# Performance work log

Hardware: AMD Instinct MI355X
Metric: run time of the kernel (lower is better)

The kernel has to match this reference:

```python
import jax, jax.numpy as jnp
import numpy as np

B, C, T, F = 16, 64, 500, 32
G = 8
GF = F // G            # 4 freqs per group
OC = GF * 64           # per-group hidden size = 256
IN = GF * C            # per-group input size = 256


def setup_inputs() -> dict:
    key = jax.random.key(0)
    k1, k2, k3, k4, k5 = jax.random.split(key, 5)
    scale = 1.0 / np.sqrt(OC)
    return {
        "x": jax.random.normal(k1, (B, C, T, F), dtype=jnp.float32),
        "weight_ih": jax.random.normal(k2, (G, 3 * OC, IN), dtype=jnp.float32) * scale,
        "weight_hh": jax.random.normal(k3, (G, 3 * OC, OC), dtype=jnp.float32) * scale,
        "bias_ih": jax.random.normal(k4, (G, 3 * OC), dtype=jnp.float32) * scale,
        "bias_hh": jax.random.normal(k5, (G, 3 * OC), dtype=jnp.float32) * scale,
    }


def reference(x, weight_ih, weight_hh, bias_ih, bias_hh):
    b, c, t, f = x.shape
    g = weight_ih.shape[0]
    oc = weight_ih.shape[1] // 3
    gf = f // g
    # [B,C,T,F] -> [B,T,F,C] -> [B,T,G,gf*C]
    xi = jnp.transpose(x, (0, 2, 3, 1)).reshape(b, t, g, gf * c)
    # input projection for all timesteps at once: [B,T,G,3*OC]
    ih = jnp.einsum('btgi,goi->btgo', xi, weight_ih) + bias_ih

    h0 = jnp.zeros((b, g, oc), dtype=x.dtype)

    def step(h, ih_t):
        hh = jnp.einsum('bgo,gpo->bgp', h, weight_hh) + bias_hh
        ri, zi, ni = jnp.split(ih_t, 3, axis=-1)
        rh, zh, nh = jnp.split(hh, 3, axis=-1)
        r = jax.nn.sigmoid(ri + rh)
        z = jax.nn.sigmoid(zi + zh)
        n = jnp.tanh(ni + r * nh)
        h_new = (1 - z) * n + z * h
        return h_new, h_new

    h_last, hs = jax.lax.scan(step, h0, jnp.swapaxes(ih, 0, 1))  # hs: [T,B,G,OC]
    out = jnp.transpose(hs, (1, 0, 2, 3))                # [B,T,G,OC]
    out = out.reshape(b, t, g, gf, oc // gf)             # unflatten OC -> (gf, out_ch)
    out = out.reshape(b, t, f, oc // gf)                 # merge (G,gf) -> F
    out = jnp.transpose(out, (0, 3, 1, 2))               # [B,out_ch,T,F]
    return out, h_last
```

## Files before the change

kernel.cpp:

```cpp
#include <hip/hip_runtime.h>

typedef _Float16 f16;
typedef _Float16 f16x2 __attribute__((ext_vector_type(2)));
typedef _Float16 f16x4 __attribute__((ext_vector_type(4)));
typedef _Float16 f16x8 __attribute__((ext_vector_type(8)));
typedef float    f32x4 __attribute__((ext_vector_type(4)));

#if defined(__has_builtin)
#if __has_builtin(__builtin_amdgcn_fdot2)
#define HAVE_FDOT2 1
#endif
#endif

__device__ __forceinline__ float dot8(f16x8 a, f16x8 b, float acc) {
#ifdef HAVE_FDOT2
  acc = __builtin_amdgcn_fdot2(__builtin_shufflevector(a, a, 0, 1),
                               __builtin_shufflevector(b, b, 0, 1), acc, false);
  acc = __builtin_amdgcn_fdot2(__builtin_shufflevector(a, a, 2, 3),
                               __builtin_shufflevector(b, b, 2, 3), acc, false);
  acc = __builtin_amdgcn_fdot2(__builtin_shufflevector(a, a, 4, 5),
                               __builtin_shufflevector(b, b, 4, 5), acc, false);
  acc = __builtin_amdgcn_fdot2(__builtin_shufflevector(a, a, 6, 7),
                               __builtin_shufflevector(b, b, 6, 7), acc, false);
#else
  #pragma unroll
  for (int i = 0; i < 8; i++) acc += (float)a[i] * (float)b[i];
#endif
  return acc;
}

__global__ void k_pack_x(const float* __restrict__ x, f16* __restrict__ xi) {
  const int tc = blockIdx.x;
  const int b  = blockIdx.y;
  const int t0 = tc * 4;
  const int tid = threadIdx.x;
  __shared__ __align__(16) float lds[64 * 133];
  #pragma unroll
  for (int it = 0; it < 32; it++) {
    int flat = it * 256 + tid;
    int c = flat >> 7;
    int t = (flat >> 5) & 3;
    int f = flat & 31;
    lds[c * 133 + t * 33 + f] =
        x[(((size_t)b * 64 + c) * 500 + t0 + t) * 32 + f];
  }
  __syncthreads();
  const int w = tid >> 6, l = tid & 63;
  #pragma unroll
  for (int rr = 0; rr < 8; rr++) {
    int row = w * 8 + rr;
    int g = row >> 2, t = row & 3;
    f16x4 v;
    #pragma unroll
    for (int e = 0; e < 4; e++) {
      int i = l * 4 + e;
      int gf = i >> 6, c = i & 63;
      v[e] = (f16)lds[c * 133 + t * 33 + g * 4 + gf];
    }
    *(f16x4*)&xi[((size_t)g * 8000 + (size_t)b * 500 + t0 + t) * 256 + l * 4] = v;
  }
}

__global__ void k_pack_wih(const float* __restrict__ w, f16* __restrict__ wh) {
  size_t i0 = ((size_t)blockIdx.x * 256 + threadIdx.x) * 8;
  f32x4 a = *(const f32x4*)(w + i0);
  f32x4 b = *(const f32x4*)(w + i0 + 4);
  f16x8 v;
  v[0]=(f16)a[0]; v[1]=(f16)a[1]; v[2]=(f16)a[2]; v[3]=(f16)a[3];
  v[4]=(f16)b[0]; v[5]=(f16)b[1]; v[6]=(f16)b[2]; v[7]=(f16)b[3];
  *(f16x8*)(wh + i0) = v;
}

__global__ void k_pack_whh(const float* __restrict__ w, f16* __restrict__ wp) {
  const int j = blockIdx.x;
  const int g = blockIdx.y;
  const int tid = threadIdx.x;
  const int row = (tid % 192) * 4 + (j >> 3);
  const int kb  = (tid / 192) * 64 + (j & 7) * 8;
  const float* src = w + ((size_t)g * 768 + row) * 256 + kb;
  f16x8 v;
  #pragma unroll
  for (int e = 0; e < 8; e++) v[e] = (f16)src[e];
  *(f16x8*)&wp[(((size_t)g * 32 + j) * 768 + tid) * 8] = v;
}

__global__ __launch_bounds__(256) void k_gemm(const f16* __restrict__ xi,
                                              const f16* __restrict__ wih,
                                              const float* __restrict__ bias,
                                              f16* __restrict__ ih) {
  const int mt = blockIdx.x;
  const int nt = blockIdx.y;
  const int g  = blockIdx.z;
  const int tid = threadIdx.x;
  const int w = tid >> 6, l = tid & 63;
  __shared__ __align__(16) f16 Als[64 * 64];
  __shared__ __align__(16) f16 Bls[128 * 64];
  f32x4 zero = {0.f, 0.f, 0.f, 0.f};
  f32x4 acc[4][2];
  #pragma unroll
  for (int mi = 0; mi < 4; mi++)
    #pragma unroll
    for (int ni = 0; ni < 2; ni++) acc[mi][ni] = zero;

  const int arow = tid >> 2, aq = tid & 3;
  const int brow = tid >> 1, bq = tid & 1;
  for (int kk = 0; kk < 4; kk++) {
    const f16* asrc = xi + ((size_t)g * 8000 + mt * 64 + arow) * 256 + kk * 64 + aq * 16;
    f16x8 a0 = *(const f16x8*)asrc;
    f16x8 a1 = *(const f16x8*)(asrc + 8);
    *(f16x8*)&Als[arow * 64 + ((aq * 2 + 0) ^ (arow & 7)) * 8] = a0;
    *(f16x8*)&Als[arow * 64 + ((aq * 2 + 1) ^ (arow & 7)) * 8] = a1;
    const f16* bsrc = wih + ((size_t)g * 768 + nt * 128 + brow) * 256 + kk * 64 + bq * 32;
    #pragma unroll
    for (int jj = 0; jj < 4; jj++) {
      f16x8 v = *(const f16x8*)(bsrc + jj * 8);
      *(f16x8*)&Bls[brow * 64 + ((bq * 4 + jj) ^ (brow & 7)) * 8] = v;
    }
    __syncthreads();
    #pragma unroll
    for (int ks = 0; ks < 2; ks++) {
      f16x8 af[4], bf[2];
      #pragma unroll
      for (int mi = 0; mi < 4; mi++) {
        int r = mi * 16 + (l & 15);
        af[mi] = *(const f16x8*)&Als[r * 64 + ((ks * 4 + (l >> 4)) ^ (r & 7)) * 8];
      }
      #pragma unroll
      for (int ni = 0; ni < 2; ni++) {
        int r = w * 32 + ni * 16 + (l & 15);
        bf[ni] = *(const f16x8*)&Bls[r * 64 + ((ks * 4 + (l >> 4)) ^ (r & 7)) * 8];
      }
      #pragma unroll
      for (int mi = 0; mi < 4; mi++)
        #pragma unroll
        for (int ni = 0; ni < 2; ni++)
          acc[mi][ni] = __builtin_amdgcn_mfma_f32_16x16x32_f16(af[mi], bf[ni], acc[mi][ni], 0, 0, 0);
    }
    __syncthreads();
  }
  #pragma unroll
  for (int ni = 0; ni < 2; ni++) {
    int col = nt * 128 + w * 32 + ni * 16 + (l & 15);
    float bs = bias[g * 768 + col];
    #pragma unroll
    for (int mi = 0; mi < 4; mi++) {
      int m0 = mt * 64 + mi * 16 + (l >> 4) * 4;
      #pragma unroll
      for (int e = 0; e < 4; e++) {
        ih[((size_t)g * 8000 + m0 + e) * 768 + col] = (f16)(acc[mi][ni][e] + bs);
      }
    }
  }
}

__global__ __launch_bounds__(768, 3) void k_recur(const f16* __restrict__ ih,
                                                  const f16* __restrict__ wp,
                                                  const float* __restrict__ bias_hh,
                                                  f16* __restrict__ hs,
                                                  float* __restrict__ hlast) {
  const int g = blockIdx.x;
  const int b = blockIdx.y;
  const int tid = threadIdx.x;
  const int kc = tid / 192;
  const int rg = tid % 192;
  __shared__ __align__(16) f16 hsm[256];
  __shared__ __align__(16) float partial[4][768];

  f16x8 wv[32];
  {
    const f16x8* src = (const f16x8*)(wp + (size_t)g * 32 * 768 * 8);
    #pragma unroll
    for (int j = 0; j < 32; j++) wv[j] = src[(size_t)j * 768 + tid];
  }
  float bh_r = 0.f, bh_z = 0.f, bh_n = 0.f;
  if (tid < 256) {
    bh_r = bias_hh[g * 768 + tid];
    bh_z = bias_hh[g * 768 + 256 + tid];
    bh_n = bias_hh[g * 768 + 512 + tid];
    hsm[tid] = (f16)0.f;
  }
  const f16* ihb = ih + ((size_t)g * 8000 + (size_t)b * 500) * 768;
  f16* hsp = hs + (size_t)(b * 8 + g) * 500 * 256;
  f16 ri = (f16)0.f, zi = (f16)0.f, nii = (f16)0.f;
  if (tid < 256) { ri = ihb[tid]; zi = ihb[256 + tid]; nii = ihb[512 + tid]; }
  __syncthreads();

  for (int t = 0; t < 500; t++) {
    f16 rin = ri, zin = zi, nin = nii;
    if (tid < 256 && t + 1 < 500) {
      const f16* p = ihb + (size_t)(t + 1) * 768;
      rin = p[tid]; zin = p[256 + tid]; nin = p[512 + tid];
    }
    float a0 = 0.f, a1 = 0.f, a2 = 0.f, a3 = 0.f;
    const f16x8* hv = (const f16x8*)(hsm + kc * 64);
    #pragma unroll
    for (int jj = 0; jj < 8; jj++) {
      f16x8 h8 = hv[jj];
      a0 = dot8(wv[jj],      h8, a0);
      a1 = dot8(wv[8 + jj],  h8, a1);
      a2 = dot8(wv[16 + jj], h8, a2);
      a3 = dot8(wv[24 + jj], h8, a3);
    }
    f32x4 p4; p4[0] = a0; p4[1] = a1; p4[2] = a2; p4[3] = a3;
    *(f32x4*)&partial[kc][rg * 4] = p4;
    __syncthreads();
    if (tid < 256) {
      const int o = tid;
      float rh = partial[0][o] + partial[1][o] + partial[2][o] + partial[3][o] + bh_r;
      float zh = partial[0][256 + o] + partial[1][256 + o] + partial[2][256 + o] + partial[3][256 + o] + bh_z;
      float nh = partial[0][512 + o] + partial[1][512 + o] + partial[2][512 + o] + partial[3][512 + o] + bh_n;
      float r = 1.f / (1.f + __expf(-((float)ri + rh)));
      float z = 1.f / (1.f + __expf(-((float)zi + zh)));
      float nx = (float)nii + r * nh;
      float n = 2.f / (1.f + __expf(-2.f * nx)) - 1.f;
      float hp = (float)hsm[o];
      float hn = (1.f - z) * n + z * hp;
      hsm[o] = (f16)hn;
      hsp[(size_t)t * 256 + o] = (f16)hn;
    }
    __syncthreads();
    ri = rin; zi = zin; nii = nin;
  }
  if (tid < 256) hlast[(size_t)(b * 8 + g) * 256 + tid] = (float)hsm[tid];
}

__global__ void k_untr(const f16* __restrict__ hs, float* __restrict__ out) {
  const int tc = blockIdx.x;
  const int b  = blockIdx.y;
  const int t0 = tc * 8;
  const int tid = threadIdx.x;
  __shared__ __align__(16) f16 lds[8 * 8 * 260];
  {
    const int row = tid >> 2, q = tid & 3;
    const int g = row >> 3, tt = row & 7;
    if (t0 + tt < 500) {
      const f16* src = hs + (((size_t)b * 8 + g) * 500 + t0 + tt) * 256 + q * 64;
      #pragma unroll
      for (int jj = 0; jj < 16; jj++) {
        *(f16x4*)&lds[(tt * 8 + g) * 260 + q * 64 + jj * 4] = *(const f16x4*)(src + jj * 4);
      }
    }
  }
  __syncthreads();
  const int w = tid >> 6, l = tid & 63;
  const int tt2 = w * 2 + (l >> 5);
  const int f = l & 31;
  const int gg = f >> 2, gf = f & 3;
  if (t0 + tt2 < 500) {
    float* dst = out + (((size_t)b * 64) * 500 + t0 + tt2) * 32 + f;
    const f16* srcl = &lds[(tt2 * 8 + gg) * 260 + gf * 64];
    #pragma unroll 4
    for (int och = 0; och < 64; och++) {
      dst[(size_t)och * 500 * 32] = (float)srcl[och];
    }
  }
}

extern "C" void kernel_launch(void* const* d_in, const int* in_sizes, int n_in,
                              void* d_out, int out_size, void* d_ws, size_t ws_size,
                              hipStream_t stream) {
  const float* x   = (const float*)d_in[0];
  const float* wih = (const float*)d_in[1];
  const float* whh = (const float*)d_in[2];
  const float* bih = (const float*)d_in[3];
  const float* bhh = (const float*)d_in[4];
  float* out   = (float*)d_out;
  float* hlast = out + 16384000;

  char* ws = (char*)d_ws;
  f16* ih_h  = (f16*)(ws);
  f16* xi_h  = (f16*)(ws + 98304000);
  f16* wih_h = (f16*)(ws + 131072000);
  f16* whh_p = (f16*)(ws + 134217728);
  f16* hs_h  = (f16*)(ws + 137363456);

  k_pack_x  <<<dim3(125, 16), 256, 0, stream>>>(x, xi_h);
  k_pack_wih<<<768, 256, 0, stream>>>(wih, wih_h);
  k_pack_whh<<<dim3(32, 8), 768, 0, stream>>>(whh, whh_p);
  k_gemm    <<<dim3(125, 6, 8), 256, 0, stream>>>(xi_h, wih_h, bih, ih_h);
  k_recur   <<<dim3(8, 16), 768, 0, stream>>>(ih_h, whh_p, bhh, hs_h, hlast);
  k_untr    <<<dim3(63, 16), 256, 0, stream>>>(hs_h, out);
}
```

Measured before the change: 682.4 us.

## Use MFMA for recurrent hidden matvec and drop cross-chunk partial reduction

The recurrent kernel now computes h·W_hh with 16x16x32 f16 MFMA instructions instead of fdot2. Only one row of each tile is used, because every row of the A operand is fed the same hidden vector. Each wave owns full-K output columns, so the four-way LDS partial-sum reduction is gone. The block shrinks from 768 to 512 threads, and W_hh is repacked into the MFMA B-operand fragment layout. The previous hidden state stays in an fp32 register instead of being reread from f16 LDS. The trade-off is that 15/16 of the MFMA work is wasted, and the per-step chain of dependent MFMAs adds latency.

```diff
diff --git a/kernel.cpp b/kernel.cpp
--- a/kernel.cpp
+++ b/kernel.cpp
@@ -1,33 +1,9 @@
 #include <hip/hip_runtime.h>
 
 typedef _Float16 f16;
-typedef _Float16 f16x2 __attribute__((ext_vector_type(2)));
 typedef _Float16 f16x4 __attribute__((ext_vector_type(4)));
 typedef _Float16 f16x8 __attribute__((ext_vector_type(8)));
 typedef float    f32x4 __attribute__((ext_vector_type(4)));
-
-#if defined(__has_builtin)
-#if __has_builtin(__builtin_amdgcn_fdot2)
-#define HAVE_FDOT2 1
-#endif
-#endif
-
-__device__ __forceinline__ float dot8(f16x8 a, f16x8 b, float acc) {
-#ifdef HAVE_FDOT2
-  acc = __builtin_amdgcn_fdot2(__builtin_shufflevector(a, a, 0, 1),
-                               __builtin_shufflevector(b, b, 0, 1), acc, false);
-  acc = __builtin_amdgcn_fdot2(__builtin_shufflevector(a, a, 2, 3),
-                               __builtin_shufflevector(b, b, 2, 3), acc, false);
-  acc = __builtin_amdgcn_fdot2(__builtin_shufflevector(a, a, 4, 5),
-                               __builtin_shufflevector(b, b, 4, 5), acc, false);
-  acc = __builtin_amdgcn_fdot2(__builtin_shufflevector(a, a, 6, 7),
-                               __builtin_shufflevector(b, b, 6, 7), acc, false);
-#else
-  #pragma unroll
-  for (int i = 0; i < 8; i++) acc += (float)a[i] * (float)b[i];
-#endif
-  return acc;
-}
 
 __global__ void k_pack_x(const float* __restrict__ x, f16* __restrict__ xi) {
   const int tc = blockIdx.x;
@@ -72,16 +48,17 @@
 }
 
 __global__ void k_pack_whh(const float* __restrict__ w, f16* __restrict__ wp) {
-  const int j = blockIdx.x;
-  const int g = blockIdx.y;
-  const int tid = threadIdx.x;
-  const int row = (tid % 192) * 4 + (j >> 3);
-  const int kb  = (tid / 192) * 64 + (j & 7) * 8;
-  const float* src = w + ((size_t)g * 768 + row) * 256 + kb;
+  const int nt = blockIdx.x;
+  const int g  = blockIdx.y;
+  const int tid = threadIdx.x;
+  const int kt = tid >> 6, l = tid & 63;
+  const int row = nt * 16 + (l & 15);
+  const int k0  = kt * 32 + ((l >> 4) & 3) * 8;
+  const float* src = w + ((size_t)g * 768 + row) * 256 + k0;
   f16x8 v;
   #pragma unroll
   for (int e = 0; e < 8; e++) v[e] = (f16)src[e];
-  *(f16x8*)&wp[(((size_t)g * 32 + j) * 768 + tid) * 8] = v;
+  *(f16x8*)&wp[((((size_t)g * 48 + nt) * 8 + kt) * 64 + l) * 8] = v;
 }
 
 __global__ __launch_bounds__(256) void k_gemm(const f16* __restrict__ xi,
@@ -153,7 +130,7 @@
   }
 }
 
-__global__ __launch_bounds__(768, 3) void k_recur(const f16* __restrict__ ih,
+__global__ __launch_bounds__(512, 2) void k_recur(const f16* __restrict__ ih,
                                                   const f16* __restrict__ wp,
                                                   const float* __restrict__ bias_hh,
                                                   f16* __restrict__ hs,
@@ -161,67 +138,87 @@
   const int g = blockIdx.x;
   const int b = blockIdx.y;
   const int tid = threadIdx.x;
-  const int kc = tid / 192;
-  const int rg = tid % 192;
+  const int w = tid >> 6, l = tid & 63;
   __shared__ __align__(16) f16 hsm[256];
-  __shared__ __align__(16) float partial[4][768];
-
-  f16x8 wv[32];
+  __shared__ __align__(16) float hhx[768];
+
+  f16x8 bf[6][8];
   {
-    const f16x8* src = (const f16x8*)(wp + (size_t)g * 32 * 768 * 8);
-    #pragma unroll
-    for (int j = 0; j < 32; j++) wv[j] = src[(size_t)j * 768 + tid];
-  }
-  float bh_r = 0.f, bh_z = 0.f, bh_n = 0.f;
+    const f16x8* wsrc = (const f16x8*)wp + (size_t)g * 48 * 8 * 64;
+    #pragma unroll
+    for (int j = 0; j < 6; j++)
+      #pragma unroll
+      for (int kt = 0; kt < 8; kt++)
+        bf[j][kt] = wsrc[(size_t)((w * 6 + j) * 8 + kt) * 64 + l];
+  }
+
+  float bh0 = 0.f, bh1 = 0.f, bh2 = 0.f, hreg = 0.f;
   if (tid < 256) {
-    bh_r = bias_hh[g * 768 + tid];
-    bh_z = bias_hh[g * 768 + 256 + tid];
-    bh_n = bias_hh[g * 768 + 512 + tid];
+    bh0 = bias_hh[g * 768 + tid];
+    bh1 = bias_hh[g * 768 + 256 + tid];
+    bh2 = bias_hh[g * 768 + 512 + tid];
     hsm[tid] = (f16)0.f;
   }
   const f16* ihb = ih + ((size_t)g * 8000 + (size_t)b * 500) * 768;
   f16* hsp = hs + (size_t)(b * 8 + g) * 500 * 256;
-  f16 ri = (f16)0.f, zi = (f16)0.f, nii = (f16)0.f;
-  if (tid < 256) { ri = ihb[tid]; zi = ihb[256 + tid]; nii = ihb[512 + tid]; }
+  f16 c0 = (f16)0.f, c1 = (f16)0.f, c2 = (f16)0.f;
+  if (tid < 256) { c0 = ihb[tid]; c1 = ihb[256 + tid]; c2 = ihb[512 + tid]; }
+  const int koff = ((l >> 4) & 3) * 8;
   __syncthreads();
 
   for (int t = 0; t < 500; t++) {
-    f16 rin = ri, zin = zi, nin = nii;
+    f16 n0 = c0, n1 = c1, n2 = c2;
     if (tid < 256 && t + 1 < 500) {
       const f16* p = ihb + (size_t)(t + 1) * 768;
-      rin = p[tid]; zin = p[256 + tid]; nin = p[512 + tid];
-    }
-    float a0 = 0.f, a1 = 0.f, a2 = 0.f, a3 = 0.f;
-    const f16x8* hv = (const f16x8*)(hsm + kc * 64);
-    #pragma unroll
-    for (int jj = 0; jj < 8; jj++) {
-      f16x8 h8 = hv[jj];
-      a0 = dot8(wv[jj],      h8, a0);
-      a1 = dot8(wv[8 + jj],  h8, a1);
-      a2 = dot8(wv[16 + jj], h8, a2);
-      a3 = dot8(wv[24 + jj], h8, a3);
-    }
-    f32x4 p4; p4[0] = a0; p4[1] = a1; p4[2] = a2; p4[3] = a3;
-    *(f32x4*)&partial[kc][rg * 4] = p4;
+      n0 = p[tid]; n1 = p[256 + tid]; n2 = p[512 + tid];
+    }
+    #pragma unroll
+    for (int half = 0; half < 2; half++) {
+      f32x4 a0 = {0.f, 0.f, 0.f, 0.f};
+      f32x4 a1 = a0, a2 = a0;
+      #pragma unroll
+      for (int hb = 0; hb < 2; hb++) {
+        f16x8 hf0 = *(const f16x8*)&hsm[(hb * 4 + 0) * 32 + koff];
+        f16x8 hf1 = *(const f16x8*)&hsm[(hb * 4 + 1) * 32 + koff];
+        f16x8 hf2 = *(const f16x8*)&hsm[(hb * 4 + 2) * 32 + koff];
+        f16x8 hf3 = *(const f16x8*)&hsm[(hb * 4 + 3) * 32 + koff];
+        a0 = __builtin_amdgcn_mfma_f32_16x16x32_f16(hf0, bf[half * 3 + 0][hb * 4 + 0], a0, 0, 0, 0);
+        a1 = __builtin_amdgcn_mfma_f32_16x16x32_f16(hf0, bf[half * 3 + 1][hb * 4 + 0], a1, 0, 0, 0);
+        a2 = __builtin_amdgcn_mfma_f32_16x16x32_f16(hf0, bf[half * 3 + 2][hb * 4 + 0], a2, 0, 0, 0);
+        a0 = __builtin_amdgcn_mfma_f32_16x16x32_f16(hf1, bf[half * 3 + 0][hb * 4 + 1], a0, 0, 0, 0);
+        a1 = __builtin_amdgcn_mfma_f32_16x16x32_f16(hf1, bf[half * 3 + 1][hb * 4 + 1], a1, 0, 0, 0);
+        a2 = __builtin_amdgcn_mfma_f32_16x16x32_f16(hf1, bf[half * 3 + 2][hb * 4 + 1], a2, 0, 0, 0);
+        a0 = __builtin_amdgcn_mfma_f32_16x16x32_f16(hf2, bf[half * 3 + 0][hb * 4 + 2], a0, 0, 0, 0);
+        a1 = __builtin_amdgcn_mfma_f32_16x16x32_f16(hf2, bf[half * 3 + 1][hb * 4 + 2], a1, 0, 0, 0);
+        a2 = __builtin_amdgcn_mfma_f32_16x16x32_f16(hf2, bf[half * 3 + 2][hb * 4 + 2], a2, 0, 0, 0);
+        a0 = __builtin_amdgcn_mfma_f32_16x16x32_f16(hf3, bf[half * 3 + 0][hb * 4 + 3], a0, 0, 0, 0);
+        a1 = __builtin_amdgcn_mfma_f32_16x16x32_f16(hf3, bf[half * 3 + 1][hb * 4 + 3], a1, 0, 0, 0);
+        a2 = __builtin_amdgcn_mfma_f32_16x16x32_f16(hf3, bf[half * 3 + 2][hb * 4 + 3], a2, 0, 0, 0);
+      }
+      if (l < 16) {
+        hhx[(w * 6 + half * 3 + 0) * 16 + l] = a0[0];
+        hhx[(w * 6 + half * 3 + 1) * 16 + l] = a1[0];
+        hhx[(w * 6 + half * 3 + 2) * 16 + l] = a2[0];
+      }
+    }
     __syncthreads();
     if (tid < 256) {
-      const int o = tid;
-      float rh = partial[0][o] + partial[1][o] + partial[2][o] + partial[3][o] + bh_r;
-      float zh = partial[0][256 + o] + partial[1][256 + o] + partial[2][256 + o] + partial[3][256 + o] + bh_z;
-      float nh = partial[0][512 + o] + partial[1][512 + o] + partial[2][512 + o] + partial[3][512 + o] + bh_n;
-      float r = 1.f / (1.f + __expf(-((float)ri + rh)));
-      float z = 1.f / (1.f + __expf(-((float)zi + zh)));
-      float nx = (float)nii + r * nh;
+      float rh = hhx[tid] + bh0;
+      float zh = hhx[256 + tid] + bh1;
+      float nh = hhx[512 + tid] + bh2;
+      float r = 1.f / (1.f + __expf(-((float)c0 + rh)));
+      float z = 1.f / (1.f + __expf(-((float)c1 + zh)));
+      float nx = (float)c2 + r * nh;
       float n = 2.f / (1.f + __expf(-2.f * nx)) - 1.f;
-      float hp = (float)hsm[o];
-      float hn = (1.f - z) * n + z * hp;
-      hsm[o] = (f16)hn;
-      hsp[(size_t)t * 256 + o] = (f16)hn;
-    }
-    __syncthreads();
-    ri = rin; zi = zin; nii = nin;
-  }
-  if (tid < 256) hlast[(size_t)(b * 8 + g) * 256 + tid] = (float)hsm[tid];
+      float hn = (1.f - z) * n + z * hreg;
+      hreg = hn;
+      hsm[tid] = (f16)hn;
+      hsp[(size_t)t * 256 + tid] = (f16)hn;
+    }
+    __syncthreads();
+    c0 = n0; c1 = n1; c2 = n2;
+  }
+  if (tid < 256) hlast[(size_t)(b * 8 + g) * 256 + tid] = hreg;
 }
 
 __global__ void k_untr(const f16* __restrict__ hs, float* __restrict__ out) {
@@ -276,8 +273,8 @@
 
   k_pack_x  <<<dim3(125, 16), 256, 0, stream>>>(x, xi_h);
   k_pack_wih<<<768, 256, 0, stream>>>(wih, wih_h);
-  k_pack_whh<<<dim3(32, 8), 768, 0, stream>>>(whh, whh_p);
+  k_pack_whh<<<dim3(48, 8), 512, 0, stream>>>(whh, whh_p);
   k_gemm    <<<dim3(125, 6, 8), 256, 0, stream>>>(xi_h, wih_h, bih, ih_h);
-  k_recur   <<<dim3(8, 16), 768, 0, stream>>>(ih_h, whh_p, bhh, hs_h, hlast);
+  k_recur   <<<dim3(8, 16), 512, 0, stream>>>(ih_h, whh_p, bhh, hs_h, hlast);
   k_untr    <<<dim3(63, 16), 256, 0, stream>>>(hs_h, out);
 }
```

New measurement: 741.3 us. 1.09x slower.

## Restructure GRU recurrence to 512 threads with shuffle reduction and one barrier

Applied to the files above, without the earlier changes.

The recurrent kernel now uses 512 threads per block. Each pair of threads owns one hidden unit across all three gates and splits the K dimension in half, combining partial sums with a lane shuffle instead of an LDS partial-sum array. The hidden state is double-buffered in LDS and also kept in a register, so each timestep needs one barrier instead of two. The cost is 48 weight vectors per thread, which raises register pressure, and twice as many threads compute the gate activations redundantly.

```diff
diff --git a/kernel.cpp b/kernel.cpp
--- a/kernel.cpp
+++ b/kernel.cpp
@@ -1,7 +1,6 @@
 #include <hip/hip_runtime.h>
 
 typedef _Float16 f16;
-typedef _Float16 f16x2 __attribute__((ext_vector_type(2)));
 typedef _Float16 f16x4 __attribute__((ext_vector_type(4)));
 typedef _Float16 f16x8 __attribute__((ext_vector_type(8)));
 typedef float    f32x4 __attribute__((ext_vector_type(4)));
@@ -75,13 +74,14 @@
   const int j = blockIdx.x;
   const int g = blockIdx.y;
   const int tid = threadIdx.x;
-  const int row = (tid % 192) * 4 + (j >> 3);
-  const int kb  = (tid / 192) * 64 + (j & 7) * 8;
-  const float* src = w + ((size_t)g * 768 + row) * 256 + kb;
+  const int q = j >> 4, kb = j & 15;
+  const int row = q * 256 + (tid >> 1);
+  const int k0  = (tid & 1) * 128 + kb * 8;
+  const float* src = w + ((size_t)g * 768 + row) * 256 + k0;
   f16x8 v;
   #pragma unroll
   for (int e = 0; e < 8; e++) v[e] = (f16)src[e];
-  *(f16x8*)&wp[(((size_t)g * 32 + j) * 768 + tid) * 8] = v;
+  *(f16x8*)&wp[(((size_t)g * 48 + j) * 512 + tid) * 8] = v;
 }
 
 __global__ __launch_bounds__(256) void k_gemm(const f16* __restrict__ xi,
@@ -153,7 +153,7 @@
   }
 }
 
-__global__ __launch_bounds__(768, 3) void k_recur(const f16* __restrict__ ih,
+__global__ __launch_bounds__(512, 2) void k_recur(const f16* __restrict__ ih,
                                                   const f16* __restrict__ wp,
                                                   const float* __restrict__ bias_hh,
                                                   f16* __restrict__ hs,
@@ -161,67 +161,61 @@
   const int g = blockIdx.x;
   const int b = blockIdx.y;
   const int tid = threadIdx.x;
-  const int kc = tid / 192;
-  const int rg = tid % 192;
-  __shared__ __align__(16) f16 hsm[256];
-  __shared__ __align__(16) float partial[4][768];
-
-  f16x8 wv[32];
+  const int r2 = tid >> 1;
+  const int kc = tid & 1;
+  __shared__ __align__(16) f16 hsm[2][256];
+
+  f16x8 wv[48];
   {
-    const f16x8* src = (const f16x8*)(wp + (size_t)g * 32 * 768 * 8);
-    #pragma unroll
-    for (int j = 0; j < 32; j++) wv[j] = src[(size_t)j * 768 + tid];
-  }
-  float bh_r = 0.f, bh_z = 0.f, bh_n = 0.f;
-  if (tid < 256) {
-    bh_r = bias_hh[g * 768 + tid];
-    bh_z = bias_hh[g * 768 + 256 + tid];
-    bh_n = bias_hh[g * 768 + 512 + tid];
-    hsm[tid] = (f16)0.f;
-  }
+    const f16x8* wsrc = (const f16x8*)wp + (size_t)g * 48 * 512;
+    #pragma unroll
+    for (int j = 0; j < 48; j++) wv[j] = wsrc[(size_t)j * 512 + tid];
+  }
+
+  const float bh0 = bias_hh[g * 768 + r2];
+  const float bh1 = bias_hh[g * 768 + 256 + r2];
+  const float bh2 = bias_hh[g * 768 + 512 + r2];
   const f16* ihb = ih + ((size_t)g * 8000 + (size_t)b * 500) * 768;
   f16* hsp = hs + (size_t)(b * 8 + g) * 500 * 256;
-  f16 ri = (f16)0.f, zi = (f16)0.f, nii = (f16)0.f;
-  if (tid < 256) { ri = ihb[tid]; zi = ihb[256 + tid]; nii = ihb[512 + tid]; }
+  float hreg = 0.f;
+  f16 c0 = ihb[r2], c1 = ihb[256 + r2], c2 = ihb[512 + r2];
+  if (tid < 256) hsm[0][tid] = (f16)0.f;
   __syncthreads();
 
+  int cur = 0;
   for (int t = 0; t < 500; t++) {
-    f16 rin = ri, zin = zi, nin = nii;
-    if (tid < 256 && t + 1 < 500) {
+    f16 n0 = c0, n1 = c1, n2 = c2;
+    if (t + 1 < 500) {
       const f16* p = ihb + (size_t)(t + 1) * 768;
-      rin = p[tid]; zin = p[256 + tid]; nin = p[512 + tid];
-    }
-    float a0 = 0.f, a1 = 0.f, a2 = 0.f, a3 = 0.f;
-    const f16x8* hv = (const f16x8*)(hsm + kc * 64);
-    #pragma unroll
-    for (int jj = 0; jj < 8; jj++) {
-      f16x8 h8 = hv[jj];
-      a0 = dot8(wv[jj],      h8, a0);
-      a1 = dot8(wv[8 + jj],  h8, a1);
-      a2 = dot8(wv[16 + jj], h8, a2);
-      a3 = dot8(wv[24 + jj], h8, a3);
-    }
-    f32x4 p4; p4[0] = a0; p4[1] = a1; p4[2] = a2; p4[3] = a3;
-    *(f32x4*)&partial[kc][rg * 4] = p4;
+      n0 = p[r2]; n1 = p[256 + r2]; n2 = p[512 + r2];
+    }
+    float a0 = 0.f, a1 = 0.f, a2 = 0.f;
+    const f16x8* hv = (const f16x8*)&hsm[cur][kc * 128];
+    #pragma unroll
+    for (int kb = 0; kb < 16; kb++) {
+      f16x8 h8 = hv[kb];
+      a0 = dot8(wv[kb],      h8, a0);
+      a1 = dot8(wv[16 + kb], h8, a1);
+      a2 = dot8(wv[32 + kb], h8, a2);
+    }
+    a0 += __shfl_xor(a0, 1, 64);
+    a1 += __shfl_xor(a1, 1, 64);
+    a2 += __shfl_xor(a2, 1, 64);
+    float r = 1.f / (1.f + __expf(-((float)c0 + a0 + bh0)));
+    float z = 1.f / (1.f + __expf(-((float)c1 + a1 + bh1)));
+    float nx = (float)c2 + r * (a2 + bh2);
+    float n = 2.f / (1.f + __expf(-2.f * nx)) - 1.f;
+    float hn = (1.f - z) * n + z * hreg;
+    hreg = hn;
+    if (kc == 0) {
+      hsm[cur ^ 1][r2] = (f16)hn;
+      hsp[(size_t)t * 256 + r2] = (f16)hn;
+    }
     __syncthreads();
-    if (tid < 256) {
-      const int o = tid;
-      float rh = partial[0][o] + partial[1][o] + partial[2][o] + partial[3][o] + bh_r;
-      float zh = partial[0][256 + o] + partial[1][256 + o] + partial[2][256 + o] + partial[3][256 + o] + bh_z;
-      float nh = partial[0][512 + o] + partial[1][512 + o] + partial[2][512 + o] + partial[3][512 + o] + bh_n;
-      float r = 1.f / (1.f + __expf(-((float)ri + rh)));
-      float z = 1.f / (1.f + __expf(-((float)zi + zh)));
-      float nx = (float)nii + r * nh;
-      float n = 2.f / (1.f + __expf(-2.f * nx)) - 1.f;
-      float hp = (float)hsm[o];
-      float hn = (1.f - z) * n + z * hp;
-      hsm[o] = (f16)hn;
-      hsp[(size_t)t * 256 + o] = (f16)hn;
-    }
-    __syncthreads();
-    ri = rin; zi = zin; nii = nin;
-  }
-  if (tid < 256) hlast[(size_t)(b * 8 + g) * 256 + tid] = (float)hsm[tid];
+    cur ^= 1;
+    c0 = n0; c1 = n1; c2 = n2;
+  }
+  if (kc == 0) hlast[(size_t)(b * 8 + g) * 256 + r2] = hreg;
 }
 
 __global__ void k_untr(const f16* __restrict__ hs, float* __restrict__ out) {
@@ -276,8 +270,8 @@
 
   k_pack_x  <<<dim3(125, 16), 256, 0, stream>>>(x, xi_h);
   k_pack_wih<<<768, 256, 0, stream>>>(wih, wih_h);
-  k_pack_whh<<<dim3(32, 8), 768, 0, stream>>>(whh, whh_p);
+  k_pack_whh<<<dim3(48, 8), 512, 0, stream>>>(whh, whh_p);
   k_gemm    <<<dim3(125, 6, 8), 256, 0, stream>>>(xi_h, wih_h, bih, ih_h);
-  k_recur   <<<dim3(8, 16), 768, 0, stream>>>(ih_h, whh_p, bhh, hs_h, hlast);
+  k_recur   <<<dim3(8, 16), 512, 0, stream>>>(ih_h, whh_p, bhh, hs_h, hlast);
   k_untr    <<<dim3(63, 16), 256, 0, stream>>>(hs_h, out);
 }
```

New measurement: 707.0 us. 3.6% more time.
